# Performance work log

Hardware: AMD Instinct MI355X
Metric: run time of the kernel (lower is better)

Reference implementation:

```python
import jax, jax.numpy as jnp
import numpy as np

B, S, H, D = 2, 8192, 16, 64
P = 8            # lsh_num_projs
BS = 256         # block_size
SAMP = 256       # sample_size


def _gray_perm(num_projs):
    # AngularLSH._unit_hamming_distance_array: maps bin ids to Gray-code order
    a = np.array([0, 1], dtype=np.int32)
    for _ in range(num_projs - 1):
        a = np.concatenate([a, np.flip(a) + a.shape[0]])
    return a

_PERM = jnp.asarray(_gray_perm(P))          # (2**P,)
_POW2 = jnp.asarray(2 ** np.arange(P), dtype=jnp.int32)


def setup_inputs() -> dict:
    rng = jax.random.key(0)
    k1, k2, k3, k4, k5 = jax.random.split(rng, 5)
    return {
        "query": jax.random.normal(k1, (B, S, H, D), jnp.float32),
        "key": jax.random.normal(k2, (B, S, H, D), jnp.float32),
        "value": jax.random.normal(k3, (B, S, H, D), jnp.float32),
        "proj_dir": jax.random.normal(k4, (D, P), jnp.float32),
        "sample_idx": jax.random.randint(k5, (B, H, SAMP), 0, S),
    }


def _lsh_hash(x, proj_dir):
    # x: (B,S,H,D) -> Gray-coded bucket ids (B,H,S)
    bits = (jnp.einsum("bshd,dp->bhsp", x, proj_dir) > 0).astype(jnp.int32)
    bins = (bits * _POW2).sum(-1)
    return _PERM[bins]


def _gather_seq(x, idx_bhs):
    # x: (B,S,H,...) gathered along seq by idx (B,H,S)
    idx = jnp.transpose(idx_bhs, (0, 2, 1))  # (B,S,H)
    if x.ndim == 4:
        idx = idx[..., None]
    return jnp.take_along_axis(x, idx, axis=1)


def reference(query, key, value, proj_dir, sample_idx):
    scale = 1.0 / float(np.sqrt(D))
    nb = S // BS

    # --- LSH sort of queries and keys (stable argsort over seq) ---
    q_sort = jnp.argsort(_lsh_hash(query, proj_dir), axis=2)   # (B,H,S)
    k_sort = jnp.argsort(_lsh_hash(key, proj_dir), axis=2)     # (B,H,S)

    q_s = _gather_seq(query, q_sort)   # (B,S,H,D)
    k_s = _gather_seq(key, k_sort)
    v_s = _gather_seq(value, k_sort)

    # --- block-diagonal attention in sorted order ---
    qb = q_s.reshape(B, nb, BS, H, D)
    kb = k_s.reshape(B, nb, BS, H, D)
    vb = v_s.reshape(B, nb, BS, H, D)
    s_blk = jnp.einsum("bnihd,bnjhd->bhnij", qb, kb) * scale   # (B,H,nb,BS,BS)
    lse_blk = jax.nn.logsumexp(s_blk, axis=-1)                 # (B,H,nb,BS)
    a_blk = jnp.einsum("bhnij,bnjhd->bnihd", jax.nn.softmax(s_blk, axis=-1), vb)
    a_blk = a_blk.reshape(B, S, H, D)                          # sorted order
    lse_blk = jnp.transpose(lse_blk, (0, 2, 3, 1)).reshape(B, S, H)

    # un-sort back to original query order
    q_inv = jnp.argsort(q_sort, axis=2)                        # inverse perm (B,H,S)
    a_blk = _gather_seq(a_blk, q_inv)                          # (B,S,H,D)
    lse_blk = _gather_seq(lse_blk, q_inv)                      # (B,S,H)

    # --- residual: uniform sampled-key attention with importance weight ---
    k_r = _gather_seq(key, sample_idx)                         # (B,SAMP,H,D)
    v_r = _gather_seq(value, sample_idx)
    s_r = jnp.einsum("bihd,bjhd->bhij", query, k_r) * scale    # (B,H,S,SAMP)
    lse_r = jax.nn.logsumexp(s_r, axis=-1) + jnp.log(S / SAMP) # (B,H,S)
    a_r = jnp.einsum("bhij,bjhd->bihd", jax.nn.softmax(s_r, axis=-1), v_r)
    lse_r = jnp.transpose(lse_r, (0, 2, 1))                    # (B,S,H)

    # --- combine block + residual estimates via log-sum-exp ---
    lse_t = jnp.logaddexp(lse_blk, lse_r)                      # (B,S,H)
    w_blk = jnp.exp(lse_blk - lse_t)[..., None]
    w_r = jnp.exp(lse_r - lse_t)[..., None]
    attn = a_blk * w_blk + a_r * w_r                           # (B,S,H,D)
    return attn
```

## Files before the change

### kernel.cpp

```cpp
#include <hip/hip_runtime.h>
#include <hip/hip_bf16.h>

#define B 2
#define S 8192
#define H 16
#define D 64
#define NB 32
#define BS 256
#define SAMP 256
#define BH (B*H)
#define BHS (B*H*S)
#define BSHD (B*S*H*D)
#define LOG32 3.4657359027997265f

typedef float f32x4 __attribute__((ext_vector_type(4)));
typedef short bf16x8 __attribute__((ext_vector_type(8)));

__device__ __forceinline__ unsigned int pack2(float a, float b) {
    unsigned int r;
    asm("v_cvt_pk_bf16_f32 %0, %1, %2" : "=v"(r) : "v"(a), "v"(b));
    return r;
}

#define HP 34

__global__ __launch_bounds__(256, 3) void k_hash(const float* __restrict__ q,
                                                 const float* __restrict__ k,
                                                 const float* __restrict__ pd,
                                                 int* __restrict__ hq,
                                                 int* __restrict__ hk,
                                                 unsigned short* __restrict__ kbf) {
    __shared__ float spd4[4 * 520];
    __shared__ unsigned int tile[256 * HP];
    __shared__ int ht[16][16];
    const int t = threadIdx.x;
    for (int i = t; i < 512; i += 256) {
        const float val = pd[i];
        spd4[i] = val; spd4[520 + i] = val;
        spd4[1040 + i] = val; spd4[1560 + i] = val;
    }
    __syncthreads();

    const bool isK = blockIdx.x >= 1024;
    const int  blk = blockIdx.x & 1023;
    const float* src = isK ? k : q;
    int* hdst = isK ? hk : hq;

    const int lane = t & 63;
    const int c    = lane & 3;
    const int rql  = (t >> 6) * 64 + (lane >> 2) * 4;
    const int rowq = blk * 256 + rql;
    const float* sp = spd4 + c * 520;

    float d[4][8];
#pragma unroll
    for (int rr = 0; rr < 4; ++rr)
#pragma unroll
        for (int p = 0; p < 8; ++p) d[rr][p] = 0.f;

#pragma unroll
    for (int j = 0; j < 4; ++j) {
        float4 x[4];
#pragma unroll
        for (int rr = 0; rr < 4; ++rr)
            x[rr] = *(const float4*)(src + ((rowq + rr) << 6) + j * 16 + c * 4);

        if (isK) {
#pragma unroll
            for (int rr = 0; rr < 4; ++rr) {
                uint2 u2;
                u2.x = pack2(x[rr].x, x[rr].y);
                u2.y = pack2(x[rr].z, x[rr].w);
                *(uint2*)&tile[(rql + rr) * HP + j * 8 + c * 2] = u2;
            }
        }
#pragma unroll
        for (int u = 0; u < 4; ++u) {
            const int dim = j * 16 + c * 4 + u;
            float4 s0 = *(const float4*)&sp[dim * 8];
            float4 s1 = *(const float4*)&sp[dim * 8 + 4];
#pragma unroll
            for (int rr = 0; rr < 4; ++rr) {
                const float xv = (u == 0) ? x[rr].x : (u == 1) ? x[rr].y
                               : (u == 2) ? x[rr].z : x[rr].w;
                d[rr][0] += xv * s0.x; d[rr][1] += xv * s0.y;
                d[rr][2] += xv * s0.z; d[rr][3] += xv * s0.w;
                d[rr][4] += xv * s1.x; d[rr][5] += xv * s1.y;
                d[rr][6] += xv * s1.z; d[rr][7] += xv * s1.w;
            }
        }
    }
#pragma unroll
    for (int rr = 0; rr < 4; ++rr)
#pragma unroll
        for (int p = 0; p < 8; ++p) {
            d[rr][p] += __shfl_xor(d[rr][p], 1);
            d[rr][p] += __shfl_xor(d[rr][p], 2);
        }
    int bits[4];
#pragma unroll
    for (int rr = 0; rr < 4; ++rr) {
        int bv = 0;
#pragma unroll
        for (int p = 0; p < 8; ++p) bv |= (d[rr][p] > 0.f) ? (1 << p) : 0;
        bits[rr] = bv;
    }
    const int myb = (c == 0) ? bits[0] : (c == 1) ? bits[1]
                  : (c == 2) ? bits[2] : bits[3];
    const int myrl = rql + c;
    ht[myrl & 15][myrl >> 4] = myb ^ (myb >> 1);
    __syncthreads();

    if (isK) {
        uint4* dst = (uint4*)(kbf + blk * 256 * 64);
#pragma unroll
        for (int it = 0; it < 8; ++it) {
            const int g = it * 256 + t;
            const unsigned int* sl = &tile[(g >> 3) * HP + (g & 7) * 4];
            uint4 val;
            val.x = sl[0]; val.y = sl[1]; val.z = sl[2]; val.w = sl[3];
            dst[g] = val;
        }
    }
    if (t < 64) {
        const int h2 = t >> 2, p2 = t & 3;
        int4 val = *(const int4*)&ht[h2][p2 * 4];
        const int gb = blk >> 9;
        const int s0 = (blk * 16) & (S - 1);
        *(int4*)&hdst[(gb * H + h2) * S + s0 + p2 * 4] = val;
    }
}

#define SORT_NT 64
#define SORT_CH (S / SORT_NT)
#define HPitch 257

__global__ __launch_bounds__(SORT_NT) void k_sort(const int* __restrict__ hq,
                                                  const int* __restrict__ hk,
                                                  int* __restrict__ qs,
                                                  int* __restrict__ ks) {
    __shared__ int hist[SORT_NT * HPitch];
    __shared__ int base[257];
    const int t  = threadIdx.x;
    const int bh = blockIdx.x & (BH - 1);
    const bool isQ = blockIdx.x < BH;
    const int* hp = (isQ ? hq : hk) + bh * S;
    int*       sp = (isQ ? qs : ks) + bh * S;

    for (int i = 0; i < HPitch; ++i) hist[t * HPitch + i] = 0;
    __syncthreads();
    for (int i = 0; i < SORT_CH; ++i) hist[t * HPitch + hp[t * SORT_CH + i]]++;
    __syncthreads();

    int v0 = 0, v1 = 0, v2 = 0, v3 = 0;
    for (int tt = 0; tt < SORT_NT; ++tt) {
        const int* hr = &hist[tt * HPitch + t * 4];
        v0 += hr[0]; v1 += hr[1]; v2 += hr[2]; v3 += hr[3];
    }
    {
        const int s1 = v0 + v1, s2 = s1 + v2, tot = s2 + v3;
        int inc = tot;
#pragma unroll
        for (int dlt = 1; dlt < 64; dlt <<= 1) {
            const int n = __shfl_up(inc, dlt);
            if (t >= dlt) inc += n;
        }
        const int ex = inc - tot;
        base[4 * t + 1] = ex + v0;
        base[4 * t + 2] = ex + s1;
        base[4 * t + 3] = ex + s2;
        base[4 * t + 4] = ex + tot;
        if (t == 0) base[0] = 0;
    }
    __syncthreads();

    for (int bi = 0; bi < 4; ++bi) {
        const int bin = t * 4 + bi;
        int run = base[bin];
        for (int tt = 0; tt < SORT_NT; ++tt) {
            int c = hist[tt * HPitch + bin];
            hist[tt * HPitch + bin] = run;
            run += c;
        }
    }
    __syncthreads();

    for (int i = 0; i < SORT_CH; ++i) {
        const int s0  = t * SORT_CH + i;
        const int bin = hp[s0];
        sp[hist[t * HPitch + bin]++] = s0;
    }
}

#define VP 264
#define PP 40

__global__ __launch_bounds__(512, 2) void k_attn(const float* __restrict__ q,
                                                 const unsigned short* __restrict__ kbf,
                                                 const float* __restrict__ v,
                                                 const int* __restrict__ qs,
                                                 const int* __restrict__ ks,
                                                 const int* __restrict__ sidx,
                                                 float* __restrict__ out) {
    __shared__ __align__(16) unsigned short vT[64 * VP];
    __shared__ __align__(16) unsigned short pL[8 * 32 * PP];

    const int t    = threadIdx.x;
    const int w    = t >> 6;
    const int lane = t & 63;
    const int lg   = lane >> 4;
    const int lr   = lane & 15;
    const int logical = (blockIdx.x & 7) * (BH * NB / 8) + (blockIdx.x >> 3);
    const int blk  = logical & (NB - 1);
    const int bh   = logical >> 5;
    const int h    = bh & (H - 1), b = bh >> 4;
    const int sbase = bh * S + blk * BS;
    unsigned short* pw = pL + w * 32 * PP;

    int qrow[2]; bf16x8 bq[2][2];
#pragma unroll
    for (int qg = 0; qg < 2; ++qg) {
        qrow[qg] = qs[sbase + w * 32 + qg * 16 + lr];
        const float* qp = q + (((b * S + qrow[qg]) * H + h) << 6);
#pragma unroll
        for (int kf = 0; kf < 2; ++kf) {
            float4 x0 = ((const float4*)(qp + kf * 32 + lg * 8))[0];
            float4 x1 = ((const float4*)(qp + kf * 32 + lg * 8))[1];
            union { bf16x8 v8; unsigned int u[4]; } fa;
            fa.u[0] = pack2(x0.x * 0.125f, x0.y * 0.125f);
            fa.u[1] = pack2(x0.z * 0.125f, x0.w * 0.125f);
            fa.u[2] = pack2(x1.x * 0.125f, x1.y * 0.125f);
            fa.u[3] = pack2(x1.z * 0.125f, x1.w * 0.125f);
            bq[qg][kf] = fa.v8;
        }
    }

    bf16x8 bv5;
    {
        union { bf16x8 v8; unsigned int u[4]; } fo;
        const unsigned int ov = (lr == 0) ? 0x3F803F80u : 0u;
        fo.u[0] = ov; fo.u[1] = ov; fo.u[2] = ov; fo.u[3] = ov;
        bv5 = fo.v8;
    }

    float m_run[2] = {-1e30f, -1e30f};
    f32x4 acc[2][4];
    f32x4 acc5[2];
#pragma unroll
    for (int qg = 0; qg < 2; ++qg) {
        acc5[qg] = (f32x4){0.f, 0.f, 0.f, 0.f};
#pragma unroll
        for (int dg = 0; dg < 4; ++dg) acc[qg][dg] = (f32x4){0.f, 0.f, 0.f, 0.f};
    }

    for (int pass = 0; pass < 2; ++pass) {
        {
            const int key = t & 255, d0 = (t >> 8) * 32;
            const int krow = pass ? sidx[bh * SAMP + key] : ks[sbase + key];
            const float* vp = v + (((b * S + krow) * H + h) << 6) + d0;
            unsigned int uv[16];
#pragma unroll
            for (int i = 0; i < 8; ++i) {
                float4 y = ((const float4*)vp)[i];
                uv[2 * i]     = pack2(y.x, y.y);
                uv[2 * i + 1] = pack2(y.z, y.w);
            }
            if (pass) __syncthreads();
#pragma unroll
            for (int j = 0; j < 16; ++j) {
                const int d = d0 + 2 * j;
                vT[(d + 0) * VP + key] = (unsigned short)(uv[j]);
                vT[(d + 1) * VP + key] = (unsigned short)(uv[j] >> 16);
            }
        }
        __syncthreads();

        const float bias = pass ? LOG32 : 0.f;

        int krw[4]; bf16x8 akp[4];
#pragma unroll
        for (int kg = 0; kg < 4; ++kg) {
            const int key = kg * 16 + lr;
            krw[kg] = pass ? sidx[bh * SAMP + key] : ks[sbase + key];
        }
#pragma unroll
        for (int kg = 0; kg < 4; ++kg)
            akp[kg] = *(const bf16x8*)(kbf + (((b * S + krw[kg]) * H + h) << 6) + lg * 8);

#pragma unroll
        for (int kt4 = 0; kt4 < 4; ++kt4) {
            bf16x8 ak1[4];
#pragma unroll
            for (int kg = 0; kg < 4; ++kg)
                ak1[kg] = *(const bf16x8*)(kbf + (((b * S + krw[kg]) * H + h) << 6)
                                           + 32 + lg * 8);
            f32x4 c[2][4];
            __builtin_amdgcn_s_setprio(1);
#pragma unroll
            for (int qg = 0; qg < 2; ++qg)
#pragma unroll
                for (int kg = 0; kg < 4; ++kg) {
                    f32x4 z = (f32x4){0.f, 0.f, 0.f, 0.f};
                    z = __builtin_amdgcn_mfma_f32_16x16x32_bf16(akp[kg], bq[qg][0], z, 0, 0, 0);
                    c[qg][kg] = __builtin_amdgcn_mfma_f32_16x16x32_bf16(ak1[kg], bq[qg][1], z, 0, 0, 0);
                }
            __builtin_amdgcn_s_setprio(0);

            int krwn[4]; bf16x8 akn[4];
            if (kt4 < 3) {
#pragma unroll
                for (int kg = 0; kg < 4; ++kg) {
                    const int key = (kt4 + 1) * 64 + kg * 16 + lr;
                    krwn[kg] = pass ? sidx[bh * SAMP + key] : ks[sbase + key];
                }
#pragma unroll
                for (int kg = 0; kg < 4; ++kg)
                    akn[kg] = *(const bf16x8*)(kbf + (((b * S + krwn[kg]) * H + h) << 6)
                                               + lg * 8);
            }

#pragma unroll
            for (int qg = 0; qg < 2; ++qg) {
                float tm = -1e30f;
#pragma unroll
                for (int kg = 0; kg < 4; ++kg)
#pragma unroll
                    for (int r = 0; r < 4; ++r) tm = fmaxf(tm, c[qg][kg][r]);
                tm = fmaxf(tm, __shfl_xor(tm, 16));
                tm = fmaxf(tm, __shfl_xor(tm, 32));
                tm += bias;
                if (!__all(tm <= m_run[qg] + 8.f)) {
                    const float mn  = fmaxf(m_run[qg], tm);
                    const float es  = __expf(m_run[qg] - mn);
                    m_run[qg] = mn;
#pragma unroll
                    for (int r = 0; r < 4; ++r) {
                        const float er = __shfl(es, lg * 4 + r);
#pragma unroll
                        for (int dg = 0; dg < 4; ++dg) acc[qg][dg][r] *= er;
                        acc5[qg][r] *= er;
                    }
                }
                const float mnb = m_run[qg] - bias;
#pragma unroll
                for (int kg = 0; kg < 4; ++kg)
#pragma unroll
                    for (int r = 0; r < 4; ++r)
                        c[qg][kg][r] = __expf(c[qg][kg][r] - mnb);
            }
#pragma unroll
            for (int hh = 0; hh < 2; ++hh) {
#pragma unroll
                for (int qg = 0; qg < 2; ++qg)
#pragma unroll
                    for (int kg2 = 0; kg2 < 2; ++kg2) {
                        const int kg = hh * 2 + kg2;
                        uint2 u;
                        u.x = pack2(c[qg][kg][0], c[qg][kg][1]);
                        u.y = pack2(c[qg][kg][2], c[qg][kg][3]);
                        *(uint2*)&pw[(qg * 16 + lr) * PP + kg2 * 16 + lg * 4] = u;
                    }
                bf16x8 bv[4];
#pragma unroll
                for (int dg = 0; dg < 4; ++dg)
                    bv[dg] = *(const bf16x8*)&vT[(dg * 16 + lr) * VP + kt4 * 64 + hh * 32 + lg * 8];
                bf16x8 ap[2];
#pragma unroll
                for (int qg = 0; qg < 2; ++qg)
                    ap[qg] = *(const bf16x8*)&pw[(qg * 16 + lr) * PP + lg * 8];
                __builtin_amdgcn_s_setprio(1);
#pragma unroll
                for (int qg = 0; qg < 2; ++qg) {
#pragma unroll
                    for (int dg = 0; dg < 4; ++dg)
                        acc[qg][dg] = __builtin_amdgcn_mfma_f32_16x16x32_bf16(ap[qg], bv[dg], acc[qg][dg], 0, 0, 0);
                    acc5[qg] = __builtin_amdgcn_mfma_f32_16x16x32_bf16(ap[qg], bv5, acc5[qg], 0, 0, 0);
                }
                __builtin_amdgcn_s_setprio(0);
            }

            if (kt4 < 3) {
#pragma unroll
                for (int kg = 0; kg < 4; ++kg) { krw[kg] = krwn[kg]; akp[kg] = akn[kg]; }
            }
        }
    }

#pragma unroll
    for (int qg = 0; qg < 2; ++qg)
#pragma unroll
        for (int r = 0; r < 4; ++r) {
            const float lq = __shfl(acc5[qg][r], lg * 16);
            const int   qr = __shfl(qrow[qg], lg * 4 + r);
            const float inv = 1.f / lq;
            const int obase = ((b * S + qr) * H + h) << 6;
#pragma unroll
            for (int dg = 0; dg < 4; ++dg)
                out[obase + dg * 16 + lr] = acc[qg][dg][r] * inv;
        }
}

extern "C" void kernel_launch(void* const* d_in, const int* in_sizes, int n_in,
                              void* d_out, int out_size, void* d_ws, size_t ws_size,
                              hipStream_t stream) {
    const float* q   = (const float*)d_in[0];
    const float* k   = (const float*)d_in[1];
    const float* v   = (const float*)d_in[2];
    const float* pd  = (const float*)d_in[3];
    const int*  sidx = (const int*)d_in[4];
    float* out = (float*)d_out;

    int* hq = (int*)d_ws;
    int* hk = hq + BHS;
    int* qs = hk + BHS;
    int* ks = qs + BHS;
    unsigned short* kbf = (unsigned short*)(ks + BHS);

    k_hash<<<2048, 256, 0, stream>>>(q, k, pd, hq, hk, kbf);
    k_sort<<<2 * BH, SORT_NT, 0, stream>>>(hq, hk, qs, ks);
    k_attn<<<BH * NB, 512, 0, stream>>>(q, kbf, v, qs, ks, sidx, out);
}
```

Before: 188.8 us.

## Drop K-prefetch registers and raise attention kernel occupancy to 3 blocks/SM

Removes the software prefetch of the next key tile's first half. The K loads now happen inside each iteration in two 32-dim halves, which reduces register pressure. It raises launch_bounds min blocks from 2 to 3 and shrinks the LDS padding for vT and pL so that three 512-thread blocks can fit per CU. The intent is to hide the gather latency through more resident waves instead of explicit prefetching. In exchange, each wave loses load/MFMA overlap, and the new LDS pitches may cause more bank conflicts.

```diff
diff --git a/kernel.cpp b/kernel.cpp
--- a/kernel.cpp
+++ b/kernel.cpp
@@ -192,10 +192,10 @@
     }
 }
 
-#define VP 264
-#define PP 40
-
-__global__ __launch_bounds__(512, 2) void k_attn(const float* __restrict__ q,
+#define VP 260
+#define PP 36
+
+__global__ __launch_bounds__(512, 3) void k_attn(const float* __restrict__ q,
                                                  const unsigned short* __restrict__ kbf,
                                                  const float* __restrict__ v,
                                                  const int* __restrict__ qs,
@@ -276,47 +276,31 @@
         __syncthreads();
 
         const float bias = pass ? LOG32 : 0.f;
-
-        int krw[4]; bf16x8 akp[4];
-#pragma unroll
-        for (int kg = 0; kg < 4; ++kg) {
-            const int key = kg * 16 + lr;
-            krw[kg] = pass ? sidx[bh * SAMP + key] : ks[sbase + key];
-        }
-#pragma unroll
-        for (int kg = 0; kg < 4; ++kg)
-            akp[kg] = *(const bf16x8*)(kbf + (((b * S + krw[kg]) * H + h) << 6) + lg * 8);
-
 #pragma unroll
         for (int kt4 = 0; kt4 < 4; ++kt4) {
-            bf16x8 ak1[4];
-#pragma unroll
-            for (int kg = 0; kg < 4; ++kg)
-                ak1[kg] = *(const bf16x8*)(kbf + (((b * S + krw[kg]) * H + h) << 6)
-                                           + 32 + lg * 8);
+            int krw[4];
+#pragma unroll
+            for (int kg = 0; kg < 4; ++kg) {
+                const int key = kt4 * 64 + kg * 16 + lr;
+                krw[kg] = pass ? sidx[bh * SAMP + key] : ks[sbase + key];
+            }
             f32x4 c[2][4];
-            __builtin_amdgcn_s_setprio(1);
-#pragma unroll
-            for (int qg = 0; qg < 2; ++qg)
-#pragma unroll
-                for (int kg = 0; kg < 4; ++kg) {
-                    f32x4 z = (f32x4){0.f, 0.f, 0.f, 0.f};
-                    z = __builtin_amdgcn_mfma_f32_16x16x32_bf16(akp[kg], bq[qg][0], z, 0, 0, 0);
-                    c[qg][kg] = __builtin_amdgcn_mfma_f32_16x16x32_bf16(ak1[kg], bq[qg][1], z, 0, 0, 0);
-                }
-            __builtin_amdgcn_s_setprio(0);
-
-            int krwn[4]; bf16x8 akn[4];
-            if (kt4 < 3) {
-#pragma unroll
-                for (int kg = 0; kg < 4; ++kg) {
-                    const int key = (kt4 + 1) * 64 + kg * 16 + lr;
-                    krwn[kg] = pass ? sidx[bh * SAMP + key] : ks[sbase + key];
-                }
+#pragma unroll
+            for (int kf = 0; kf < 2; ++kf) {
+                bf16x8 ak[4];
 #pragma unroll
                 for (int kg = 0; kg < 4; ++kg)
-                    akn[kg] = *(const bf16x8*)(kbf + (((b * S + krwn[kg]) * H + h) << 6)
-                                               + lg * 8);
+                    ak[kg] = *(const bf16x8*)(kbf + (((b * S + krw[kg]) * H + h) << 6)
+                                              + kf * 32 + lg * 8);
+                __builtin_amdgcn_s_setprio(1);
+#pragma unroll
+                for (int qg = 0; qg < 2; ++qg)
+#pragma unroll
+                    for (int kg = 0; kg < 4; ++kg) {
+                        f32x4 cin = kf ? c[qg][kg] : (f32x4){0.f, 0.f, 0.f, 0.f};
+                        c[qg][kg] = __builtin_amdgcn_mfma_f32_16x16x32_bf16(ak[kg], bq[qg][kf], cin, 0, 0, 0);
+                    }
+                __builtin_amdgcn_s_setprio(0);
             }
 
 #pragma unroll
@@ -377,11 +361,6 @@
                     acc5[qg] = __builtin_amdgcn_mfma_f32_16x16x32_bf16(ap[qg], bv5, acc5[qg], 0, 0, 0);
                 }
                 __builtin_amdgcn_s_setprio(0);
-            }
-
-            if (kt4 < 3) {
-#pragma unroll
-                for (int kg = 0; kg < 4; ++kg) { krw[kg] = krwn[kg]; akp[kg] = akn[kg]; }
             }
         }
     }
```

Result: slower. 204.9 us (+8.5%).
